# Kernel tuning notes

Measured on AMD Instinct MI355X. Metric: run time of the kernel, lower is better.

## Reference

```python
import jax, jax.numpy as jnp
import numpy as np

B, T, D, FF, H, K = 8, 1024, 512, 2048, 8, 15
HD = D // H  # key_dim = d_model // num_heads


def _ln(x, g, b):
    # keras LayerNormalization default epsilon = 1e-3
    m = jnp.mean(x, axis=-1, keepdims=True)
    v = jnp.var(x, axis=-1, keepdims=True)
    return (x - m) * jax.lax.rsqrt(v + 1e-3) * g + b


def setup_inputs() -> dict:
    key = jax.random.key(0)
    ks = iter(jax.random.split(key, 64))

    def rn(shape, s=0.02):
        return jax.random.normal(next(ks), shape, jnp.float32) * s

    p = {}
    p['x'] = jax.random.normal(next(ks), (B, T, D), jnp.float32)
    # ff_pre: LN -> Dense(FF, relu) -> Dense(D)
    p['g1'] = jnp.ones((D,), jnp.float32); p['b1'] = jnp.zeros((D,), jnp.float32)
    p['Wff1'] = rn((D, FF)); p['bff1'] = jnp.zeros((FF,), jnp.float32)
    p['Wff2'] = rn((FF, D)); p['bff2'] = jnp.zeros((D,), jnp.float32)
    # attention norm + MHA projections (keras EinsumDense shapes)
    p['ga'] = jnp.ones((D,), jnp.float32); p['ba'] = jnp.zeros((D,), jnp.float32)
    p['Wq'] = rn((D, H, HD)); p['bq'] = jnp.zeros((H, HD), jnp.float32)
    p['Wk'] = rn((D, H, HD)); p['bk'] = jnp.zeros((H, HD), jnp.float32)
    p['Wv'] = rn((D, H, HD)); p['bv'] = jnp.zeros((H, HD), jnp.float32)
    p['Wo'] = rn((H, HD, D)); p['bo'] = jnp.zeros((D,), jnp.float32)
    # conv branch: LN -> pointwise conv (2D, gelu) -> depthwise conv(k=15) -> BN -> swish -> pointwise conv (D)
    p['gc'] = jnp.ones((D,), jnp.float32); p['bc'] = jnp.zeros((D,), jnp.float32)
    p['Wcp'] = rn((D, 2 * D)); p['bcp'] = jnp.zeros((2 * D,), jnp.float32)
    p['dwk'] = rn((K, 1, 2 * D)); p['dwb'] = jnp.zeros((2 * D,), jnp.float32)
    p['bn_g'] = jnp.ones((2 * D,), jnp.float32); p['bn_b'] = jnp.zeros((2 * D,), jnp.float32)
    p['bn_m'] = jnp.zeros((2 * D,), jnp.float32)
    p['bn_v'] = jnp.ones((2 * D,), jnp.float32)
    p['Wco'] = rn((2 * D, D)); p['bco'] = jnp.zeros((D,), jnp.float32)
    # ff_post
    p['g2'] = jnp.ones((D,), jnp.float32); p['b2'] = jnp.zeros((D,), jnp.float32)
    p['Wf1'] = rn((D, FF)); p['bf1'] = jnp.zeros((FF,), jnp.float32)
    p['Wf2'] = rn((FF, D)); p['bf2'] = jnp.zeros((D,), jnp.float32)
    return p


def reference(x, g1, b1, Wff1, bff1, Wff2, bff2, ga, ba, Wq, bq, Wk, bk, Wv, bv, Wo, bo, gc, bc, Wcp, bcp, dwk, dwb, bn_g, bn_b, bn_m, bn_v, Wco, bco, g2, b2, Wf1, bf1, Wf2, bf2):
    # Macaron FFN (pre), half-step residual applied later
    x_ff = jnp.maximum(_ln(x, g1, b1) @ Wff1 + bff1, 0.0) @ Wff2 + bff2

    # causal multi-head self-attention (cache=None path)
    a = _ln(x, ga, ba)
    q = jnp.einsum('btd,dhk->bthk', a, Wq) + bq
    k = jnp.einsum('btd,dhk->bthk', a, Wk) + bk
    v = jnp.einsum('btd,dhk->bthk', a, Wv) + bv
    scores = jnp.einsum('bqhd,bkhd->bhqk', q, k) / jnp.sqrt(jnp.float32(HD))
    causal = jnp.tril(jnp.ones((T, T), bool))  # [T,T]
    scores = jnp.where(causal, scores, jnp.float32(-1e9))
    w = jax.nn.softmax(scores, axis=-1)
    ctx = jnp.einsum('bhqk,bkhd->bqhd', w, v)
    attn = jnp.einsum('bqhd,hdo->bqo', ctx, Wo) + bo

    x = x + 0.5 * x_ff + attn

    # convolution module: pointwise(gelu) -> causal left-pad -> depthwise -> BN(inference) -> swish -> pointwise
    c = jax.nn.gelu(_ln(x, gc, bc) @ Wcp + bcp, approximate=False)
    c = jnp.pad(c, ((0, 0), (K - 1, 0), (0, 0)))  # causal pad
    c = jax.lax.conv_general_dilated(
        c, dwk, window_strides=(1,), padding='VALID',
        dimension_numbers=('NWC', 'WIO', 'NWC'), feature_group_count=2 * D) + dwb
    c = (c - bn_m) * jax.lax.rsqrt(bn_v + 1e-3) * bn_g + bn_b
    c = c * jax.nn.sigmoid(c)  # swish
    c = c @ Wco + bco
    x = x + c

    # post FFN (full residual)
    x = x + (jnp.maximum(_ln(x, g2, b2) @ Wf1 + bf1, 0.0) @ Wf2 + bf2)
    return x
```

## Files before the change

### kernel.cpp

```cpp
#include <hip/hip_runtime.h>
#include <hip/hip_bf16.h>
#include <math.h>

#define BB 8
#define TT 1024
#define DD 512
#define FFD 2048
#define HH 8
#define HDD 64
#define KW 15
#define MR (BB*TT)
#define QKVN 1536

typedef __attribute__((ext_vector_type(8))) short short8;
typedef __attribute__((ext_vector_type(4))) short short4v;
typedef __attribute__((ext_vector_type(4))) float f32x4;
typedef __hip_bfloat16 bf16;

__device__ __forceinline__ float bf2f(unsigned u16) {
    return __uint_as_float(u16 << 16);
}

__device__ __forceinline__ void async_copy16(const void* g, void* l) {
    __builtin_amdgcn_global_load_lds(
        (const __attribute__((address_space(1))) void*)g,
        (__attribute__((address_space(3))) void*)l, 16, 0, 0);
}

__device__ __forceinline__ float gelu_exact(float v) {
    return 0.5f * v * (1.0f + erff(v * 0.70710678118654752f));
}

__global__ __launch_bounds__(256) void ln_dual_kernel(const float* __restrict__ x,
                                                      const float* __restrict__ g1,
                                                      const float* __restrict__ b1,
                                                      const float* __restrict__ ga,
                                                      const float* __restrict__ ba,
                                                      bf16* __restrict__ o1,
                                                      bf16* __restrict__ o2) {
    int wave = (blockIdx.x * blockDim.x + threadIdx.x) >> 6;
    int lane = threadIdx.x & 63;
    if (wave >= MR) return;
    const float* row = x + (size_t)wave * DD;
    float4 v0 = ((const float4*)row)[lane];
    float4 v1 = ((const float4*)row)[64 + lane];
    float s  = v0.x + v0.y + v0.z + v0.w + v1.x + v1.y + v1.z + v1.w;
    float ss = v0.x*v0.x + v0.y*v0.y + v0.z*v0.z + v0.w*v0.w
             + v1.x*v1.x + v1.y*v1.y + v1.z*v1.z + v1.w*v1.w;
    #pragma unroll
    for (int off = 32; off >= 1; off >>= 1) {
        s  += __shfl_xor(s,  off, 64);
        ss += __shfl_xor(ss, off, 64);
    }
    float mean = s * (1.0f / DD);
    float var  = ss * (1.0f / DD) - mean * mean;
    float r    = rsqrtf(var + 1e-3f);
    float n0x = (v0.x - mean) * r, n0y = (v0.y - mean) * r,
          n0z = (v0.z - mean) * r, n0w = (v0.w - mean) * r;
    float n1x = (v1.x - mean) * r, n1y = (v1.y - mean) * r,
          n1z = (v1.z - mean) * r, n1w = (v1.w - mean) * r;
    {
        float4 g0 = ((const float4*)g1)[lane];
        float4 gg1 = ((const float4*)g1)[64 + lane];
        float4 b0 = ((const float4*)b1)[lane];
        float4 bb1 = ((const float4*)b1)[64 + lane];
        alignas(8) bf16 oo0[4], oo1[4];
        oo0[0] = __float2bfloat16(n0x * g0.x + b0.x);
        oo0[1] = __float2bfloat16(n0y * g0.y + b0.y);
        oo0[2] = __float2bfloat16(n0z * g0.z + b0.z);
        oo0[3] = __float2bfloat16(n0w * g0.w + b0.w);
        oo1[0] = __float2bfloat16(n1x * gg1.x + bb1.x);
        oo1[1] = __float2bfloat16(n1y * gg1.y + bb1.y);
        oo1[2] = __float2bfloat16(n1z * gg1.z + bb1.z);
        oo1[3] = __float2bfloat16(n1w * gg1.w + bb1.w);
        bf16* orow = o1 + (size_t)wave * DD;
        *(short4v*)(orow + lane * 4)       = *(const short4v*)oo0;
        *(short4v*)(orow + 256 + lane * 4) = *(const short4v*)oo1;
    }
    {
        float4 g0 = ((const float4*)ga)[lane];
        float4 gg1 = ((const float4*)ga)[64 + lane];
        float4 b0 = ((const float4*)ba)[lane];
        float4 bb1 = ((const float4*)ba)[64 + lane];
        alignas(8) bf16 oo0[4], oo1[4];
        oo0[0] = __float2bfloat16(n0x * g0.x + b0.x);
        oo0[1] = __float2bfloat16(n0y * g0.y + b0.y);
        oo0[2] = __float2bfloat16(n0z * g0.z + b0.z);
        oo0[3] = __float2bfloat16(n0w * g0.w + b0.w);
        oo1[0] = __float2bfloat16(n1x * gg1.x + bb1.x);
        oo1[1] = __float2bfloat16(n1y * gg1.y + bb1.y);
        oo1[2] = __float2bfloat16(n1z * gg1.z + bb1.z);
        oo1[3] = __float2bfloat16(n1w * gg1.w + bb1.w);
        bf16* orow = o2 + (size_t)wave * DD;
        *(short4v*)(orow + lane * 4)       = *(const short4v*)oo0;
        *(short4v*)(orow + 256 + lane * 4) = *(const short4v*)oo1;
    }
}

__global__ __launch_bounds__(256) void ln_kernel(const float* __restrict__ x,
                                                 const float* __restrict__ g,
                                                 const float* __restrict__ b,
                                                 bf16* __restrict__ out) {
    int wave = (blockIdx.x * blockDim.x + threadIdx.x) >> 6;
    int lane = threadIdx.x & 63;
    if (wave >= MR) return;
    const float* row = x + (size_t)wave * DD;
    float4 v0 = ((const float4*)row)[lane];
    float4 v1 = ((const float4*)row)[64 + lane];
    float s  = v0.x + v0.y + v0.z + v0.w + v1.x + v1.y + v1.z + v1.w;
    float ss = v0.x*v0.x + v0.y*v0.y + v0.z*v0.z + v0.w*v0.w
             + v1.x*v1.x + v1.y*v1.y + v1.z*v1.z + v1.w*v1.w;
    #pragma unroll
    for (int off = 32; off >= 1; off >>= 1) {
        s  += __shfl_xor(s,  off, 64);
        ss += __shfl_xor(ss, off, 64);
    }
    float mean = s * (1.0f / DD);
    float var  = ss * (1.0f / DD) - mean * mean;
    float r    = rsqrtf(var + 1e-3f);
    float4 g0 = ((const float4*)g)[lane];
    float4 g1 = ((const float4*)g)[64 + lane];
    float4 b0 = ((const float4*)b)[lane];
    float4 b1 = ((const float4*)b)[64 + lane];
    alignas(8) bf16 o0[4], o1[4];
    o0[0] = __float2bfloat16((v0.x - mean) * r * g0.x + b0.x);
    o0[1] = __float2bfloat16((v0.y - mean) * r * g0.y + b0.y);
    o0[2] = __float2bfloat16((v0.z - mean) * r * g0.z + b0.z);
    o0[3] = __float2bfloat16((v0.w - mean) * r * g0.w + b0.w);
    o1[0] = __float2bfloat16((v1.x - mean) * r * g1.x + b1.x);
    o1[1] = __float2bfloat16((v1.y - mean) * r * g1.y + b1.y);
    o1[2] = __float2bfloat16((v1.z - mean) * r * g1.z + b1.z);
    o1[3] = __float2bfloat16((v1.w - mean) * r * g1.w + b1.w);
    bf16* orow = out + (size_t)wave * DD;
    *(short4v*)(orow + lane * 4)       = *(const short4v*)o0;
    *(short4v*)(orow + 256 + lane * 4) = *(const short4v*)o1;
}

struct WtPack {
    const float* src[10];
    bf16*        dst[10];
    int          K[10];
    int          lgNT[10];
    float        scale[10];
    int          off[10];
    const float* bq; const float* bk; const float* bv;
    float*       bdst;
};

__global__ __launch_bounds__(256) void wtrans_all_kernel(WtPack P) {
    __shared__ alignas(16) bf16 T[64][72];
    const int bid = blockIdx.x;
    if (bid >= 1536) {
        #pragma unroll
        for (int it = 0; it < 6; ++it) {
            int i = it * 256 + threadIdx.x;
            float v = i < 512 ? P.bq[i] * 0.125f
                              : (i < 1024 ? P.bk[i - 512] : P.bv[i - 1024]);
            P.bdst[i] = v;
        }
        return;
    }
    int e = 0;
    #pragma unroll
    for (int i = 1; i < 10; ++i) e = (bid >= P.off[i]) ? i : e;
    const float* W  = P.src[e];
    bf16*        Wt = P.dst[e];
    const int    K  = P.K[e];
    const int    lg = P.lgNT[e];
    const float  scale = P.scale[e];
    const int local = bid - P.off[e];
    const int bx = local & ((1 << lg) - 1);
    const int by = local >> lg;
    const int k0 = by * 64;
    const int n0 = bx * 64;
    const int N  = (1 << lg) * 64;
    const int tid = threadIdx.x;
    #pragma unroll
    for (int it = 0; it < 4; ++it) {
        int lin = it * 256 + tid;
        int kl  = lin >> 4;
        int nq  = (lin & 15) * 4;
        float4 v = *(const float4*)(W + (size_t)(k0 + kl) * N + n0 + nq);
        T[nq + 0][kl] = __float2bfloat16(v.x * scale);
        T[nq + 1][kl] = __float2bfloat16(v.y * scale);
        T[nq + 2][kl] = __float2bfloat16(v.z * scale);
        T[nq + 3][kl] = __float2bfloat16(v.w * scale);
    }
    __syncthreads();
    #pragma unroll
    for (int it = 0; it < 4; ++it) {
        int lin = it * 256 + tid;
        int nl  = lin >> 4;
        int kq  = (lin & 15) * 4;
        *(short4v*)(Wt + (size_t)(n0 + nl) * K + k0 + kq) = *(const short4v*)&T[nl][kq];
    }
}

template<int BN, int OP, int RESMODE, int OUTMODE>
__global__ __launch_bounds__(256) void bgemm_kernel(
    const bf16* __restrict__ A,
    const bf16* __restrict__ Bt,
    const float* __restrict__ bias,
    const float* __restrict__ res1,
    const bf16* __restrict__ res2,
    bf16* __restrict__ aux,
    float s2, float oscale,
    void* __restrict__ Cout,
    int N, int Kd, int nxb)
{
    constexpr int NT = BN / 32;
    __shared__ alignas(16) bf16 As[128][64];
    __shared__ alignas(16) bf16 Bs[BN][64];
    const int tid  = threadIdx.x;
    const int w    = tid >> 6;
    const int lane = tid & 63;
    const int quad = lane >> 4;
    const int l16  = lane & 15;
    const int wm   = w >> 1, wn = w & 1;

    const int flat = blockIdx.x;
    const int c8   = flat & 7;
    const int j    = flat >> 3;
    const int jy   = j / nxb;
    const int m0   = (c8 * 8 + jy) * 128;
    const int n0   = (j - jy * nxb) * BN;

    const int srow = lane >> 3;
    const int scol = ((lane & 7) ^ srow) * 8;

    const bf16* Ap = A  + (size_t)(m0 + w * 32 + srow) * Kd + scol;
    const bf16* Bp = Bt + (size_t)(n0 + w * (BN / 4) + srow) * Kd + scol;

    f32x4 acc[4][NT] = {};

    for (int k0 = 0; k0 < Kd; k0 += 64) {
        #pragma unroll
        for (int i = 0; i < 4; ++i)
            async_copy16(Ap + (size_t)(i * 8) * Kd + k0, &As[w * 32 + i * 8][0]);
        #pragma unroll
        for (int i = 0; i < BN / 32; ++i)
            async_copy16(Bp + (size_t)(i * 8) * Kd + k0, &Bs[w * (BN / 4) + i * 8][0]);
        __syncthreads();
        #pragma unroll
        for (int ks = 0; ks < 2; ++ks) {
            short8 af[4], bfr[NT];
            #pragma unroll
            for (int mt = 0; mt < 4; ++mt) {
                const int row = wm * 64 + mt * 16 + l16;
                const int c   = ((ks * 4 + quad) ^ (row & 7)) * 16;
                af[mt] = *(const short8*)((const char*)&As[row][0] + c);
            }
            #pragma unroll
            for (int nt = 0; nt < NT; ++nt) {
                const int col = wn * (BN / 2) + nt * 16 + l16;
                const int c   = ((ks * 4 + quad) ^ (col & 7)) * 16;
                bfr[nt] = *(const short8*)((const char*)&Bs[col][0] + c);
            }
            #pragma unroll
            for (int mt = 0; mt < 4; ++mt)
                #pragma unroll
                for (int nt = 0; nt < NT; ++nt)
                    acc[mt][nt] = __builtin_amdgcn_mfma_f32_16x16x32_bf16(
                        af[mt], bfr[nt], acc[mt][nt], 0, 0, 0);
        }
        __syncthreads();
    }

    const int crow0 = m0 + wm * 64 + quad * 4;
    const int ccol0 = n0 + wn * (BN / 2) + l16;
    #pragma unroll
    for (int nt = 0; nt < NT; ++nt) {
        const int col = ccol0 + nt * 16;
        const float bv = bias[col];
        #pragma unroll
        for (int mt = 0; mt < 4; ++mt) {
            if (OUTMODE == 2) {
                alignas(8) bf16 o4[4];
                #pragma unroll
                for (int r = 0; r < 4; ++r)
                    o4[r] = __float2bfloat16((acc[mt][nt][r] + bv) * oscale);
                if (col < 1024) {
                    #pragma unroll
                    for (int r = 0; r < 4; ++r)
                        ((bf16*)Cout)[(size_t)(crow0 + mt * 16 + r) * N + col] = o4[r];
                } else {
                    const int dg   = col - 1024;
                    const int rowt = crow0 + mt * 16;
                    const int b2   = rowt >> 10, t0 = rowt & 1023;
                    const int bh2  = b2 * 8 + (dg >> 6), d = dg & 63;
                    *(short4v*)(aux + ((size_t)bh2 * 64 + d) * TT + t0) =
                        *(const short4v*)o4;
                }
            } else {
                #pragma unroll
                for (int r = 0; r < 4; ++r) {
                    const int row = crow0 + mt * 16 + r;
                    const size_t off = (size_t)row * N + col;
                    float o = acc[mt][nt][r] + bv;
                    if (OP == 1)      o = fmaxf(o, 0.f);
                    else if (OP == 2) o = gelu_exact(o);
                    if (RESMODE >= 1) o += res1[off];
                    if (RESMODE == 2) o += s2 * __bfloat162float(res2[off]);
                    if (OUTMODE == 0) ((float*)Cout)[off] = o;
                    else              ((bf16*)Cout)[off]  = __float2bfloat16(o * oscale);
                }
            }
        }
    }
}

__global__ __launch_bounds__(256) void fattn_kernel(
    const bf16* __restrict__ QKV,
    const bf16* __restrict__ Vt,
    bf16* __restrict__ ctx)
{
    __shared__ alignas(16) bf16 Ks[2][64][64];
    __shared__ alignas(16) bf16 Vs[2][64][64];
    const int tid  = threadIdx.x;
    const int w    = tid >> 6;
    const int lane = tid & 63;
    const int quad = lane >> 4;
    const int l16  = lane & 15;
    const int bh   = blockIdx.x & 63;
    const int bi   = 7 - (blockIdx.x >> 6);
    const int b = bh >> 3, h = bh & 7;

    const bf16* Qg = QKV + (size_t)(b * TT) * QKVN + h * 64;
    const bf16* Kg = QKV + (size_t)(b * TT) * QKVN + 512 + h * 64;
    const bf16* Vg = Vt  + (size_t)bh * 64 * TT;

    const int qL = bi * 128 + w * 16;
    const int qH = qL + 64;
    short8 qfL0 = *(const short8*)(Qg + (size_t)(qL + l16) * QKVN + quad * 8);
    short8 qfL1 = *(const short8*)(Qg + (size_t)(qL + l16) * QKVN + 32 + quad * 8);
    short8 qfH0 = *(const short8*)(Qg + (size_t)(qH + l16) * QKVN + quad * 8);
    short8 qfH1 = *(const short8*)(Qg + (size_t)(qH + l16) * QKVN + 32 + quad * 8);

    const int sgrow  = lane >> 3;
    const int sgchnk = lane & 7;

    f32x4 caccL[4] = {}, caccH[4] = {};
    float lL = 0.f, lH = 0.f;
    const int prow_base = ((l16 >> 2) << 3) + (l16 & 3);
    const int smax = 2 * bi + 1;

    #pragma unroll
    for (int i = 0; i < 2; ++i) {
        const int rowbase = w * 8 + i * 32;
        const int row = rowbase + sgrow;
        const int fR = (row & 3) | (((row >> 3) & 1) << 2);
        const int sc = sgchnk ^ fR;
        async_copy16(Kg + (size_t)row * QKVN + sc * 8, &Ks[0][rowbase][0]);
        async_copy16(Vg + (size_t)row * TT + sc * 8,   &Vs[0][rowbase][0]);
    }

    int buf = 0;
    for (int s = 0; s <= smax; ++s) {
        __syncthreads();
        if (s < smax) {
            const int kn = (s + 1) * 64;
            #pragma unroll
            for (int i = 0; i < 2; ++i) {
                const int rowbase = w * 8 + i * 32;
                const int row = rowbase + sgrow;
                const int fR = (row & 3) | (((row >> 3) & 1) << 2);
                const int sc = sgchnk ^ fR;
                async_copy16(Kg + (size_t)(kn + row) * QKVN + sc * 8, &Ks[buf ^ 1][rowbase][0]);
                async_copy16(Vg + (size_t)row * TT + kn + sc * 8,     &Vs[buf ^ 1][rowbase][0]);
            }
        }
        const int k0 = s * 64;
        const bool doL = (s < smax);

        f32x4 sTL[4], sTH[4];
        #pragma unroll
        for (int s4 = 0; s4 < 4; ++s4) {
            const int prow = prow_base + (s4 >> 1) * 32 + (s4 & 1) * 4;
            const int fR = (prow & 3) | (((prow >> 3) & 1) << 2);
            short8 ka = *(const short8*)&Ks[buf][prow][(quad ^ fR) * 8];
            short8 kb = *(const short8*)&Ks[buf][prow][((4 + quad) ^ fR) * 8];
            f32x4 zH = {0.f, 0.f, 0.f, 0.f};
            zH = __builtin_amdgcn_mfma_f32_16x16x32_bf16(ka, qfH0, zH, 0, 0, 0);
            sTH[s4] = __builtin_amdgcn_mfma_f32_16x16x32_bf16(kb, qfH1, zH, 0, 0, 0);
            if (doL) {
                f32x4 zL = {0.f, 0.f, 0.f, 0.f};
                zL = __builtin_amdgcn_mfma_f32_16x16x32_bf16(ka, qfL0, zL, 0, 0, 0);
                sTL[s4] = __builtin_amdgcn_mfma_f32_16x16x32_bf16(kb, qfL1, zL, 0, 0, 0);
            }
        }

        alignas(16) bf16 pbH[16], pbL[16];
        if (s == smax) {
            const int qg = qH + l16;
            #pragma unroll
            for (int s4 = 0; s4 < 4; ++s4)
                #pragma unroll
                for (int r = 0; r < 4; ++r) {
                    const int key = k0 + (s4 >> 1) * 32 + quad * 8 + (s4 & 1) * 4 + r;
                    const float p = (key <= qg) ? __expf(sTH[s4][r]) : 0.f;
                    lH += p;
                    pbH[s4 * 4 + r] = __float2bfloat16(p);
                }
        } else {
            #pragma unroll
            for (int s4 = 0; s4 < 4; ++s4)
                #pragma unroll
                for (int r = 0; r < 4; ++r) {
                    const float p = __expf(sTH[s4][r]);
                    lH += p;
                    pbH[s4 * 4 + r] = __float2bfloat16(p);
                }
        }
        if (doL) {
            if (s == smax - 1) {
                const int qg = qL + l16;
                #pragma unroll
                for (int s4 = 0; s4 < 4; ++s4)
                    #pragma unroll
                    for (int r = 0; r < 4; ++r) {
                        const int key = k0 + (s4 >> 1) * 32 + quad * 8 + (s4 & 1) * 4 + r;
                        const float p = (key <= qg) ? __expf(sTL[s4][r]) : 0.f;
                        lL += p;
                        pbL[s4 * 4 + r] = __float2bfloat16(p);
                    }
            } else {
                #pragma unroll
                for (int s4 = 0; s4 < 4; ++s4)
                    #pragma unroll
                    for (int r = 0; r < 4; ++r) {
                        const float p = __expf(sTL[s4][r]);
                        lL += p;
                        pbL[s4 * 4 + r] = __float2bfloat16(p);
                    }
            }
        }
        const short8 pfH0 = *(const short8*)&pbH[0];
        const short8 pfH1 = *(const short8*)&pbH[8];
        const short8 pfL0 = *(const short8*)&pbL[0];
        const short8 pfL1 = *(const short8*)&pbL[8];

        #pragma unroll
        for (int g = 0; g < 4; ++g) {
            const int vrow = g * 16 + l16;
            const int fR = (vrow & 3) | (((vrow >> 3) & 1) << 2);
            short8 va = *(const short8*)&Vs[buf][vrow][(quad ^ fR) * 8];
            short8 vb = *(const short8*)&Vs[buf][vrow][((4 + quad) ^ fR) * 8];
            caccH[g] = __builtin_amdgcn_mfma_f32_16x16x32_bf16(va, pfH0, caccH[g], 0, 0, 0);
            caccH[g] = __builtin_amdgcn_mfma_f32_16x16x32_bf16(vb, pfH1, caccH[g], 0, 0, 0);
            if (doL) {
                caccL[g] = __builtin_amdgcn_mfma_f32_16x16x32_bf16(va, pfL0, caccL[g], 0, 0, 0);
                caccL[g] = __builtin_amdgcn_mfma_f32_16x16x32_bf16(vb, pfL1, caccL[g], 0, 0, 0);
            }
        }
        buf ^= 1;
    }

    lL += __shfl_xor(lL, 16, 64);
    lL += __shfl_xor(lL, 32, 64);
    lH += __shfl_xor(lH, 16, 64);
    lH += __shfl_xor(lH, 32, 64);
    const float invL = 1.0f / lL;
    const float invH = 1.0f / lH;

    bf16* CbL = ctx + (size_t)(b * TT + qL + l16) * DD + h * 64;
    bf16* CbH = ctx + (size_t)(b * TT + qH + l16) * DD + h * 64;
    #pragma unroll
    for (int g = 0; g < 4; ++g) {
        alignas(8) bf16 oL[4], oH[4];
        #pragma unroll
        for (int r = 0; r < 4; ++r) {
            oL[r] = __float2bfloat16(caccL[g][r] * invL);
            oH[r] = __float2bfloat16(caccH[g][r] * invH);
        }
        *(short4v*)(CbL + g * 16 + quad * 4) = *(const short4v*)oL;
        *(short4v*)(CbH + g * 16 + quad * 4) = *(const short4v*)oH;
    }
}

__global__ __launch_bounds__(256) void dwconv_kernel(const bf16* __restrict__ c1,
                                                     const float* __restrict__ dwk,
                                                     const float* __restrict__ dwb,
                                                     const float* __restrict__ bn_g,
                                                     const float* __restrict__ bn_b,
                                                     const float* __restrict__ bn_m,
                                                     const float* __restrict__ bn_v,
                                                     bf16* __restrict__ out) {
    const int C2 = 2 * DD;
    const int lin = blockIdx.x * 256 + threadIdx.x;
    const int chp = lin & 511;
    const int ch  = chp << 1;
    const int tch = lin >> 9;
    const int row0 = tch << 3;
    const int t0   = row0 & (TT - 1);

    float w0[KW], w1[KW];
    #pragma unroll
    for (int i = 0; i < KW; ++i) {
        w0[i] = dwk[i * C2 + ch];
        w1[i] = dwk[i * C2 + ch + 1];
    }
    const float a0 = rsqrtf(bn_v[ch] + 1e-3f) * bn_g[ch];
    const float a1 = rsqrtf(bn_v[ch + 1] + 1e-3f) * bn_g[ch + 1];
    const float c0 = (dwb[ch] - bn_m[ch]) * a0 + bn_b[ch];
    const float c1v = (dwb[ch + 1] - bn_m[ch + 1]) * a1 + bn_b[ch + 1];

    float x0[22], x1[22];
    if (t0 >= KW - 1) {
        #pragma unroll
        for (int i = 0; i < 22; ++i) {
            unsigned u = *(const unsigned*)(c1 + (size_t)(row0 - (KW - 1) + i) * C2 + ch);
            x0[i] = bf2f(u & 0xffff);
            x1[i] = bf2f(u >> 16);
        }
    } else {
        #pragma unroll
        for (int i = 0; i < 22; ++i) {
            unsigned u = 0;
            if (t0 - (KW - 1) + i >= 0)
                u = *(const unsigned*)(c1 + (size_t)(row0 - (KW - 1) + i) * C2 + ch);
            x0[i] = bf2f(u & 0xffff);
            x1[i] = bf2f(u >> 16);
        }
    }

    #pragma unroll
    for (int j = 0; j < 8; ++j) {
        float s0 = 0.f, s1 = 0.f;
        #pragma unroll
        for (int i = 0; i < KW; ++i) {
            s0 += x0[j + i] * w0[i];
            s1 += x1[j + i] * w1[i];
        }
        s0 = s0 * a0 + c0;
        s1 = s1 * a1 + c1v;
        s0 = s0 / (1.f + __expf(-s0));
        s1 = s1 / (1.f + __expf(-s1));
        alignas(4) bf16 ob[2] = {__float2bfloat16(s0), __float2bfloat16(s1)};
        *(unsigned*)(out + (size_t)(row0 + j) * C2 + ch) = *(const unsigned*)ob;
    }
}

extern "C" void kernel_launch(void* const* d_in, const int* in_sizes, int n_in,
                              void* d_out, int out_size, void* d_ws, size_t ws_size,
                              hipStream_t stream) {
    const float* x    = (const float*)d_in[0];
    const float* g1   = (const float*)d_in[1];
    const float* b1   = (const float*)d_in[2];
    const float* Wff1 = (const float*)d_in[3];
    const float* bff1 = (const float*)d_in[4];
    const float* Wff2 = (const float*)d_in[5];
    const float* bff2 = (const float*)d_in[6];
    const float* ga   = (const float*)d_in[7];
    const float* ba   = (const float*)d_in[8];
    const float* Wq   = (const float*)d_in[9];
    const float* bq   = (const float*)d_in[10];
    const float* Wk   = (const float*)d_in[11];
    const float* bk   = (const float*)d_in[12];
    const float* Wv   = (const float*)d_in[13];
    const float* bv   = (const float*)d_in[14];
    const float* Wo   = (const float*)d_in[15];
    const float* bo   = (const float*)d_in[16];
    const float* gc   = (const float*)d_in[17];
    const float* bc   = (const float*)d_in[18];
    const float* Wcp  = (const float*)d_in[19];
    const float* bcp  = (const float*)d_in[20];
    const float* dwk  = (const float*)d_in[21];
    const float* dwb  = (const float*)d_in[22];
    const float* bn_g = (const float*)d_in[23];
    const float* bn_b = (const float*)d_in[24];
    const float* bn_m = (const float*)d_in[25];
    const float* bn_v = (const float*)d_in[26];
    const float* Wco  = (const float*)d_in[27];
    const float* bco  = (const float*)d_in[28];
    const float* g2   = (const float*)d_in[29];
    const float* b2   = (const float*)d_in[30];
    const float* Wf1  = (const float*)d_in[31];
    const float* bf1  = (const float*)d_in[32];
    const float* Wf2  = (const float*)d_in[33];
    const float* bf2  = (const float*)d_in[34];

    float* out = (float*)d_out;

    char* p = (char*)d_ws;
    bf16* lnb   = (bf16*)p;  p += (size_t)MR * DD * 2;
    bf16* lnab  = (bf16*)p;  p += (size_t)MR * DD * 2;
    bf16* qkvb  = (bf16*)p;  p += (size_t)MR * QKVN * 2;
    bf16* Vtb   = (bf16*)p;  p += (size_t)MR * DD * 2;
    bf16* ctxb  = (bf16*)p;  p += (size_t)MR * DD * 2;
    bf16* xffb  = (bf16*)p;  p += (size_t)MR * DD * 2;
    bf16* bigb  = (bf16*)p;  p += (size_t)MR * FFD * 2;
    bf16* c2b   = (bf16*)p;  p += (size_t)MR * 1024 * 2;
    bf16* Wff1t = (bf16*)p;  p += (size_t)FFD * DD * 2;
    bf16* Wff2t = (bf16*)p;  p += (size_t)DD * FFD * 2;
    bf16* Wqkvt = (bf16*)p;  p += (size_t)QKVN * DD * 2;
    bf16* Wot   = (bf16*)p;  p += (size_t)DD * DD * 2;
    bf16* Wcpt  = (bf16*)p;  p += (size_t)1024 * DD * 2;
    bf16* Wcot  = (bf16*)p;  p += (size_t)DD * 1024 * 2;
    bf16* Wf1t  = (bf16*)p;  p += (size_t)FFD * DD * 2;
    bf16* Wf2t  = (bf16*)p;  p += (size_t)DD * FFD * 2;
    float* bqkv = (float*)p; p += QKVN * 4;

    dim3 blk(256);
    dim3 ln_grid(MR / 4);

    WtPack P;
    auto set = [&](int i, const float* s, bf16* d, int K, int N, float sc, int off) {
        P.src[i] = s; P.dst[i] = d; P.K[i] = K; P.scale[i] = sc; P.off[i] = off;
        int nt = N / 64, lg = 0; while ((1 << lg) < nt) ++lg; P.lgNT[i] = lg;
    };
    set(0, Wff1, Wff1t, DD,  FFD, 1.f,    0);
    set(1, Wff2, Wff2t, FFD, DD,  1.f,    256);
    set(2, Wq,   Wqkvt,                DD, DD, 0.125f, 512);
    set(3, Wk,   Wqkvt + (size_t)512 * DD,  DD, DD, 1.f, 576);
    set(4, Wv,   Wqkvt + (size_t)1024 * DD, DD, DD, 1.f, 640);
    set(5, Wo,   Wot,   DD,  DD,  1.f,    704);
    set(6, Wcp,  Wcpt,  DD,  1024, 1.f,   768);
    set(7, Wco,  Wcot,  1024, DD, 1.f,    896);
    set(8, Wf1,  Wf1t,  DD,  FFD, 1.f,    1024);
    set(9, Wf2,  Wf2t,  FFD, DD,  1.f,    1280);
    P.bq = bq; P.bk = bk; P.bv = bv; P.bdst = bqkv;
    wtrans_all_kernel<<<dim3(1537), blk, 0, stream>>>(P);

    ln_dual_kernel<<<ln_grid, blk, 0, stream>>>(x, g1, b1, ga, ba, lnb, lnab);
    bgemm_kernel<128, 1, 0, 1><<<dim3(16 * 64), blk, 0, stream>>>(
        lnb, Wff1t, bff1, nullptr, nullptr, nullptr, 0.f, 1.f, bigb, FFD, DD, 16);
    bgemm_kernel<64, 0, 0, 1><<<dim3(8 * 64), blk, 0, stream>>>(
        bigb, Wff2t, bff2, nullptr, nullptr, nullptr, 0.f, 1.f, xffb, DD, FFD, 8);
    bgemm_kernel<128, 0, 0, 2><<<dim3(12 * 64), blk, 0, stream>>>(
        lnab, Wqkvt, bqkv, nullptr, nullptr, Vtb, 0.f, 1.f, qkvb, QKVN, DD, 12);
    fattn_kernel<<<dim3(64 * 8), blk, 0, stream>>>(qkvb, Vtb, ctxb);
    bgemm_kernel<64, 0, 2, 0><<<dim3(8 * 64), blk, 0, stream>>>(
        ctxb, Wot, bo, x, xffb, nullptr, 0.5f, 1.f, out, DD, DD, 8);
    ln_kernel<<<ln_grid, blk, 0, stream>>>(out, gc, bc, lnb);
    bgemm_kernel<128, 2, 0, 1><<<dim3(8 * 64), blk, 0, stream>>>(
        lnb, Wcpt, bcp, nullptr, nullptr, nullptr, 0.f, 1.f, bigb, 1024, DD, 8);
    dwconv_kernel<<<dim3(MR * 512 / 8 / 256), blk, 0, stream>>>(
        bigb, dwk, dwb, bn_g, bn_b, bn_m, bn_v, c2b);
    bgemm_kernel<64, 0, 1, 0><<<dim3(8 * 64), blk, 0, stream>>>(
        c2b, Wcot, bco, out, nullptr, nullptr, 0.f, 1.f, out, DD, 1024, 8);
    ln_kernel<<<ln_grid, blk, 0, stream>>>(out, g2, b2, lnb);
    bgemm_kernel<128, 1, 0, 1><<<dim3(16 * 64), blk, 0, stream>>>(
        lnb, Wf1t, bf1, nullptr, nullptr, nullptr, 0.f, 1.f, bigb, FFD, DD, 16);
    bgemm_kernel<64, 0, 1, 0><<<dim3(8 * 64), blk, 0, stream>>>(
        bigb, Wf2t, bf2, out, nullptr, nullptr, 0.f, 1.f, out, DD, FFD, 8);
}
```

Before: 394.7 us.

## Merge independent stages into combined multi-job kernels to cut launches and idle tails

Folds the dual LayerNorm into the weight-transpose prep kernel and runs FF1 and QKV GEMMs in one launch by splitting blocks by index. It also runs the FF2 GEMM alongside flash attention in one kernel. Independent work can then fill the device together and fewer launches occur. The cost is heterogeneous blocks sharing one register and LDS budget, which may lower occupancy for the attention and GEMM paths.

```diff
diff --git a/kernel.cpp b/kernel.cpp
--- a/kernel.cpp
+++ b/kernel.cpp
@@ -31,112 +31,7 @@
     return 0.5f * v * (1.0f + erff(v * 0.70710678118654752f));
 }
 
-__global__ __launch_bounds__(256) void ln_dual_kernel(const float* __restrict__ x,
-                                                      const float* __restrict__ g1,
-                                                      const float* __restrict__ b1,
-                                                      const float* __restrict__ ga,
-                                                      const float* __restrict__ ba,
-                                                      bf16* __restrict__ o1,
-                                                      bf16* __restrict__ o2) {
-    int wave = (blockIdx.x * blockDim.x + threadIdx.x) >> 6;
-    int lane = threadIdx.x & 63;
-    if (wave >= MR) return;
-    const float* row = x + (size_t)wave * DD;
-    float4 v0 = ((const float4*)row)[lane];
-    float4 v1 = ((const float4*)row)[64 + lane];
-    float s  = v0.x + v0.y + v0.z + v0.w + v1.x + v1.y + v1.z + v1.w;
-    float ss = v0.x*v0.x + v0.y*v0.y + v0.z*v0.z + v0.w*v0.w
-             + v1.x*v1.x + v1.y*v1.y + v1.z*v1.z + v1.w*v1.w;
-    #pragma unroll
-    for (int off = 32; off >= 1; off >>= 1) {
-        s  += __shfl_xor(s,  off, 64);
-        ss += __shfl_xor(ss, off, 64);
-    }
-    float mean = s * (1.0f / DD);
-    float var  = ss * (1.0f / DD) - mean * mean;
-    float r    = rsqrtf(var + 1e-3f);
-    float n0x = (v0.x - mean) * r, n0y = (v0.y - mean) * r,
-          n0z = (v0.z - mean) * r, n0w = (v0.w - mean) * r;
-    float n1x = (v1.x - mean) * r, n1y = (v1.y - mean) * r,
-          n1z = (v1.z - mean) * r, n1w = (v1.w - mean) * r;
-    {
-        float4 g0 = ((const float4*)g1)[lane];
-        float4 gg1 = ((const float4*)g1)[64 + lane];
-        float4 b0 = ((const float4*)b1)[lane];
-        float4 bb1 = ((const float4*)b1)[64 + lane];
-        alignas(8) bf16 oo0[4], oo1[4];
-        oo0[0] = __float2bfloat16(n0x * g0.x + b0.x);
-        oo0[1] = __float2bfloat16(n0y * g0.y + b0.y);
-        oo0[2] = __float2bfloat16(n0z * g0.z + b0.z);
-        oo0[3] = __float2bfloat16(n0w * g0.w + b0.w);
-        oo1[0] = __float2bfloat16(n1x * gg1.x + bb1.x);
-        oo1[1] = __float2bfloat16(n1y * gg1.y + bb1.y);
-        oo1[2] = __float2bfloat16(n1z * gg1.z + bb1.z);
-        oo1[3] = __float2bfloat16(n1w * gg1.w + bb1.w);
-        bf16* orow = o1 + (size_t)wave * DD;
-        *(short4v*)(orow + lane * 4)       = *(const short4v*)oo0;
-        *(short4v*)(orow + 256 + lane * 4) = *(const short4v*)oo1;
-    }
-    {
-        float4 g0 = ((const float4*)ga)[lane];
-        float4 gg1 = ((const float4*)ga)[64 + lane];
-        float4 b0 = ((const float4*)ba)[lane];
-        float4 bb1 = ((const float4*)ba)[64 + lane];
-        alignas(8) bf16 oo0[4], oo1[4];
-        oo0[0] = __float2bfloat16(n0x * g0.x + b0.x);
-        oo0[1] = __float2bfloat16(n0y * g0.y + b0.y);
-        oo0[2] = __float2bfloat16(n0z * g0.z + b0.z);
-        oo0[3] = __float2bfloat16(n0w * g0.w + b0.w);
-        oo1[0] = __float2bfloat16(n1x * gg1.x + bb1.x);
-        oo1[1] = __float2bfloat16(n1y * gg1.y + bb1.y);
-        oo1[2] = __float2bfloat16(n1z * gg1.z + bb1.z);
-        oo1[3] = __float2bfloat16(n1w * gg1.w + bb1.w);
-        bf16* orow = o2 + (size_t)wave * DD;
-        *(short4v*)(orow + lane * 4)       = *(const short4v*)oo0;
-        *(short4v*)(orow + 256 + lane * 4) = *(const short4v*)oo1;
-    }
-}
-
-__global__ __launch_bounds__(256) void ln_kernel(const float* __restrict__ x,
-                                                 const float* __restrict__ g,
-                                                 const float* __restrict__ b,
-                                                 bf16* __restrict__ out) {
-    int wave = (blockIdx.x * blockDim.x + threadIdx.x) >> 6;
-    int lane = threadIdx.x & 63;
-    if (wave >= MR) return;
-    const float* row = x + (size_t)wave * DD;
-    float4 v0 = ((const float4*)row)[lane];
-    float4 v1 = ((const float4*)row)[64 + lane];
-    float s  = v0.x + v0.y + v0.z + v0.w + v1.x + v1.y + v1.z + v1.w;
-    float ss = v0.x*v0.x + v0.y*v0.y + v0.z*v0.z + v0.w*v0.w
-             + v1.x*v1.x + v1.y*v1.y + v1.z*v1.z + v1.w*v1.w;
-    #pragma unroll
-    for (int off = 32; off >= 1; off >>= 1) {
-        s  += __shfl_xor(s,  off, 64);
-        ss += __shfl_xor(ss, off, 64);
-    }
-    float mean = s * (1.0f / DD);
-    float var  = ss * (1.0f / DD) - mean * mean;
-    float r    = rsqrtf(var + 1e-3f);
-    float4 g0 = ((const float4*)g)[lane];
-    float4 g1 = ((const float4*)g)[64 + lane];
-    float4 b0 = ((const float4*)b)[lane];
-    float4 b1 = ((const float4*)b)[64 + lane];
-    alignas(8) bf16 o0[4], o1[4];
-    o0[0] = __float2bfloat16((v0.x - mean) * r * g0.x + b0.x);
-    o0[1] = __float2bfloat16((v0.y - mean) * r * g0.y + b0.y);
-    o0[2] = __float2bfloat16((v0.z - mean) * r * g0.z + b0.z);
-    o0[3] = __float2bfloat16((v0.w - mean) * r * g0.w + b0.w);
-    o1[0] = __float2bfloat16((v1.x - mean) * r * g1.x + b1.x);
-    o1[1] = __float2bfloat16((v1.y - mean) * r * g1.y + b1.y);
-    o1[2] = __float2bfloat16((v1.z - mean) * r * g1.z + b1.z);
-    o1[3] = __float2bfloat16((v1.w - mean) * r * g1.w + b1.w);
-    bf16* orow = out + (size_t)wave * DD;
-    *(short4v*)(orow + lane * 4)       = *(const short4v*)o0;
-    *(short4v*)(orow + 256 + lane * 4) = *(const short4v*)o1;
-}
-
-struct WtPack {
+struct PrepPack {
     const float* src[10];
     bf16*        dst[10];
     int          K[10];
@@ -145,18 +40,80 @@
     int          off[10];
     const float* bq; const float* bk; const float* bv;
     float*       bdst;
+    const float* x;
+    const float* g1; const float* b1; const float* ga; const float* ba;
+    bf16* o1; bf16* o2;
 };
 
-__global__ __launch_bounds__(256) void wtrans_all_kernel(WtPack P) {
+__global__ __launch_bounds__(256) void prep_kernel(PrepPack P) {
     __shared__ alignas(16) bf16 T[64][72];
     const int bid = blockIdx.x;
-    if (bid >= 1536) {
+    if (bid == 1536) {
         #pragma unroll
         for (int it = 0; it < 6; ++it) {
             int i = it * 256 + threadIdx.x;
             float v = i < 512 ? P.bq[i] * 0.125f
                               : (i < 1024 ? P.bk[i - 512] : P.bv[i - 1024]);
             P.bdst[i] = v;
+        }
+        return;
+    }
+    if (bid > 1536) {
+        int wave = ((bid - 1537) * 256 + (int)threadIdx.x) >> 6;
+        int lane = threadIdx.x & 63;
+        const float* row = P.x + (size_t)wave * DD;
+        float4 v0 = ((const float4*)row)[lane];
+        float4 v1 = ((const float4*)row)[64 + lane];
+        float s  = v0.x + v0.y + v0.z + v0.w + v1.x + v1.y + v1.z + v1.w;
+        float ss = v0.x*v0.x + v0.y*v0.y + v0.z*v0.z + v0.w*v0.w
+                 + v1.x*v1.x + v1.y*v1.y + v1.z*v1.z + v1.w*v1.w;
+        #pragma unroll
+        for (int off = 32; off >= 1; off >>= 1) {
+            s  += __shfl_xor(s,  off, 64);
+            ss += __shfl_xor(ss, off, 64);
+        }
+        float mean = s * (1.0f / DD);
+        float var  = ss * (1.0f / DD) - mean * mean;
+        float r    = rsqrtf(var + 1e-3f);
+        float n0x = (v0.x - mean) * r, n0y = (v0.y - mean) * r,
+              n0z = (v0.z - mean) * r, n0w = (v0.w - mean) * r;
+        float n1x = (v1.x - mean) * r, n1y = (v1.y - mean) * r,
+              n1z = (v1.z - mean) * r, n1w = (v1.w - mean) * r;
+        {
+            float4 g0 = ((const float4*)P.g1)[lane];
+            float4 gg = ((const float4*)P.g1)[64 + lane];
+            float4 b0 = ((const float4*)P.b1)[lane];
+            float4 bb = ((const float4*)P.b1)[64 + lane];
+            alignas(8) bf16 o0[4], o1[4];
+            o0[0] = __float2bfloat16(n0x * g0.x + b0.x);
+            o0[1] = __float2bfloat16(n0y * g0.y + b0.y);
+            o0[2] = __float2bfloat16(n0z * g0.z + b0.z);
+            o0[3] = __float2bfloat16(n0w * g0.w + b0.w);
+            o1[0] = __float2bfloat16(n1x * gg.x + bb.x);
+            o1[1] = __float2bfloat16(n1y * gg.y + bb.y);
+            o1[2] = __float2bfloat16(n1z * gg.z + bb.z);
+            o1[3] = __float2bfloat16(n1w * gg.w + bb.w);
+            bf16* orow = P.o1 + (size_t)wave * DD;
+            *(short4v*)(orow + lane * 4)       = *(const short4v*)o0;
+            *(short4v*)(orow + 256 + lane * 4) = *(const short4v*)o1;
+        }
+        {
+            float4 g0 = ((const float4*)P.ga)[lane];
+            float4 gg = ((const float4*)P.ga)[64 + lane];
+            float4 b0 = ((const float4*)P.ba)[lane];
+            float4 bb = ((const float4*)P.ba)[64 + lane];
+            alignas(8) bf16 o0[4], o1[4];
+            o0[0] = __float2bfloat16(n0x * g0.x + b0.x);
+            o0[1] = __float2bfloat16(n0y * g0.y + b0.y);
+            o0[2] = __float2bfloat16(n0z * g0.z + b0.z);
+            o0[3] = __float2bfloat16(n0w * g0.w + b0.w);
+            o1[0] = __float2bfloat16(n1x * gg.x + bb.x);
+            o1[1] = __float2bfloat16(n1y * gg.y + bb.y);
+            o1[2] = __float2bfloat16(n1z * gg.z + bb.z);
+            o1[3] = __float2bfloat16(n1w * gg.w + bb.w);
+            bf16* orow = P.o2 + (size_t)wave * DD;
+            *(short4v*)(orow + lane * 4)       = *(const short4v*)o0;
+            *(short4v*)(orow + 256 + lane * 4) = *(const short4v*)o1;
         }
         return;
     }
@@ -196,6 +153,45 @@
     }
 }
 
+__global__ __launch_bounds__(256) void ln_kernel(const float* __restrict__ x,
+                                                 const float* __restrict__ g,
+                                                 const float* __restrict__ b,
+                                                 bf16* __restrict__ out) {
+    int wave = (blockIdx.x * blockDim.x + threadIdx.x) >> 6;
+    int lane = threadIdx.x & 63;
+    if (wave >= MR) return;
+    const float* row = x + (size_t)wave * DD;
+    float4 v0 = ((const float4*)row)[lane];
+    float4 v1 = ((const float4*)row)[64 + lane];
+    float s  = v0.x + v0.y + v0.z + v0.w + v1.x + v1.y + v1.z + v1.w;
+    float ss = v0.x*v0.x + v0.y*v0.y + v0.z*v0.z + v0.w*v0.w
+             + v1.x*v1.x + v1.y*v1.y + v1.z*v1.z + v1.w*v1.w;
+    #pragma unroll
+    for (int off = 32; off >= 1; off >>= 1) {
+        s  += __shfl_xor(s,  off, 64);
+        ss += __shfl_xor(ss, off, 64);
+    }
+    float mean = s * (1.0f / DD);
+    float var  = ss * (1.0f / DD) - mean * mean;
+    float r    = rsqrtf(var + 1e-3f);
+    float4 g0 = ((const float4*)g)[lane];
+    float4 g1 = ((const float4*)g)[64 + lane];
+    float4 b0 = ((const float4*)b)[lane];
+    float4 b1 = ((const float4*)b)[64 + lane];
+    alignas(8) bf16 o0[4], o1[4];
+    o0[0] = __float2bfloat16((v0.x - mean) * r * g0.x + b0.x);
+    o0[1] = __float2bfloat16((v0.y - mean) * r * g0.y + b0.y);
+    o0[2] = __float2bfloat16((v0.z - mean) * r * g0.z + b0.z);
+    o0[3] = __float2bfloat16((v0.w - mean) * r * g0.w + b0.w);
+    o1[0] = __float2bfloat16((v1.x - mean) * r * g1.x + b1.x);
+    o1[1] = __float2bfloat16((v1.y - mean) * r * g1.y + b1.y);
+    o1[2] = __float2bfloat16((v1.z - mean) * r * g1.z + b1.z);
+    o1[3] = __float2bfloat16((v1.w - mean) * r * g1.w + b1.w);
+    bf16* orow = out + (size_t)wave * DD;
+    *(short4v*)(orow + lane * 4)       = *(const short4v*)o0;
+    *(short4v*)(orow + 256 + lane * 4) = *(const short4v*)o1;
+}
+
 template<int BN, int OP, int RESMODE, int OUTMODE>
 __global__ __launch_bounds__(256) void bgemm_kernel(
     const bf16* __restrict__ A,
@@ -203,7 +199,6 @@
     const float* __restrict__ bias,
     const float* __restrict__ res1,
     const bf16* __restrict__ res2,
-    bf16* __restrict__ aux,
     float s2, float oscale,
     void* __restrict__ Cout,
     int N, int Kd, int nxb)
@@ -274,206 +269,370 @@
         const float bv = bias[col];
         #pragma unroll
         for (int mt = 0; mt < 4; ++mt) {
-            if (OUTMODE == 2) {
-                alignas(8) bf16 o4[4];
-                #pragma unroll
-                for (int r = 0; r < 4; ++r)
-                    o4[r] = __float2bfloat16((acc[mt][nt][r] + bv) * oscale);
-                if (col < 1024) {
-                    #pragma unroll
-                    for (int r = 0; r < 4; ++r)
-                        ((bf16*)Cout)[(size_t)(crow0 + mt * 16 + r) * N + col] = o4[r];
-                } else {
-                    const int dg   = col - 1024;
-                    const int rowt = crow0 + mt * 16;
-                    const int b2   = rowt >> 10, t0 = rowt & 1023;
-                    const int bh2  = b2 * 8 + (dg >> 6), d = dg & 63;
-                    *(short4v*)(aux + ((size_t)bh2 * 64 + d) * TT + t0) =
-                        *(const short4v*)o4;
-                }
-            } else {
-                #pragma unroll
-                for (int r = 0; r < 4; ++r) {
-                    const int row = crow0 + mt * 16 + r;
-                    const size_t off = (size_t)row * N + col;
-                    float o = acc[mt][nt][r] + bv;
-                    if (OP == 1)      o = fmaxf(o, 0.f);
-                    else if (OP == 2) o = gelu_exact(o);
-                    if (RESMODE >= 1) o += res1[off];
-                    if (RESMODE == 2) o += s2 * __bfloat162float(res2[off]);
-                    if (OUTMODE == 0) ((float*)Cout)[off] = o;
-                    else              ((bf16*)Cout)[off]  = __float2bfloat16(o * oscale);
-                }
-            }
-        }
-    }
-}
-
-__global__ __launch_bounds__(256) void fattn_kernel(
-    const bf16* __restrict__ QKV,
-    const bf16* __restrict__ Vt,
-    bf16* __restrict__ ctx)
+            #pragma unroll
+            for (int r = 0; r < 4; ++r) {
+                const int row = crow0 + mt * 16 + r;
+                const size_t off = (size_t)row * N + col;
+                float o = acc[mt][nt][r] + bv;
+                if (OP == 1)      o = fmaxf(o, 0.f);
+                else if (OP == 2) o = gelu_exact(o);
+                if (RESMODE >= 1) o += res1[off];
+                if (RESMODE == 2) o += s2 * __bfloat162float(res2[off]);
+                if (OUTMODE == 0) ((float*)Cout)[off] = o;
+                else              ((bf16*)Cout)[off]  = __float2bfloat16(o * oscale);
+            }
+        }
+    }
+}
+
+__global__ __launch_bounds__(256) void ffqkv_kernel(
+    const bf16* __restrict__ lnb, const bf16* __restrict__ lnab,
+    const bf16* __restrict__ Wff1t, const bf16* __restrict__ Wqkvt,
+    const float* __restrict__ bff1, const float* __restrict__ bqkv,
+    bf16* __restrict__ bigb, bf16* __restrict__ qkvb, bf16* __restrict__ Vtb)
 {
-    __shared__ alignas(16) bf16 Ks[2][64][64];
-    __shared__ alignas(16) bf16 Vs[2][64][64];
+    __shared__ alignas(16) bf16 As[128][64];
+    __shared__ alignas(16) bf16 Bs[128][64];
     const int tid  = threadIdx.x;
     const int w    = tid >> 6;
     const int lane = tid & 63;
     const int quad = lane >> 4;
     const int l16  = lane & 15;
-    const int bh   = blockIdx.x & 63;
-    const int bi   = 7 - (blockIdx.x >> 6);
-    const int b = bh >> 3, h = bh & 7;
-
-    const bf16* Qg = QKV + (size_t)(b * TT) * QKVN + h * 64;
-    const bf16* Kg = QKV + (size_t)(b * TT) * QKVN + 512 + h * 64;
-    const bf16* Vg = Vt  + (size_t)bh * 64 * TT;
-
-    const int qL = bi * 128 + w * 16;
-    const int qH = qL + 64;
-    short8 qfL0 = *(const short8*)(Qg + (size_t)(qL + l16) * QKVN + quad * 8);
-    short8 qfL1 = *(const short8*)(Qg + (size_t)(qL + l16) * QKVN + 32 + quad * 8);
-    short8 qfH0 = *(const short8*)(Qg + (size_t)(qH + l16) * QKVN + quad * 8);
-    short8 qfH1 = *(const short8*)(Qg + (size_t)(qH + l16) * QKVN + 32 + quad * 8);
-
-    const int sgrow  = lane >> 3;
-    const int sgchnk = lane & 7;
-
-    f32x4 caccL[4] = {}, caccH[4] = {};
-    float lL = 0.f, lH = 0.f;
-    const int prow_base = ((l16 >> 2) << 3) + (l16 & 3);
-    const int smax = 2 * bi + 1;
-
+    const int wm   = w >> 1, wn = w & 1;
+
+    const bool jobq = blockIdx.x >= 1024;
+    const int  flat = jobq ? (int)blockIdx.x - 1024 : (int)blockIdx.x;
+    const int  nxb  = jobq ? 12 : 16;
+    const int  N    = jobq ? QKVN : FFD;
+    const bf16* A   = jobq ? lnab : lnb;
+    const bf16* Bt  = jobq ? Wqkvt : Wff1t;
+    const float* bias = jobq ? bqkv : bff1;
+
+    const int c8 = flat & 7;
+    const int j  = flat >> 3;
+    const int jy = j / nxb;
+    const int m0 = (c8 * 8 + jy) * 128;
+    const int n0 = (j - jy * nxb) * 128;
+
+    const int srow = lane >> 3;
+    const int scol = ((lane & 7) ^ srow) * 8;
+
+    const bf16* Ap = A  + (size_t)(m0 + w * 32 + srow) * DD + scol;
+    const bf16* Bp = Bt + (size_t)(n0 + w * 32 + srow) * DD + scol;
+
+    f32x4 acc[4][4] = {};
+
+    for (int k0 = 0; k0 < DD; k0 += 64) {
+        #pragma unroll
+        for (int i = 0; i < 4; ++i) {
+            async_copy16(Ap + (size_t)(i * 8) * DD + k0, &As[w * 32 + i * 8][0]);
+            async_copy16(Bp + (size_t)(i * 8) * DD + k0, &Bs[w * 32 + i * 8][0]);
+        }
+        __syncthreads();
+        #pragma unroll
+        for (int ks = 0; ks < 2; ++ks) {
+            short8 af[4], bfr[4];
+            #pragma unroll
+            for (int mt = 0; mt < 4; ++mt) {
+                const int row = wm * 64 + mt * 16 + l16;
+                const int c   = ((ks * 4 + quad) ^ (row & 7)) * 16;
+                af[mt] = *(const short8*)((const char*)&As[row][0] + c);
+            }
+            #pragma unroll
+            for (int nt = 0; nt < 4; ++nt) {
+                const int col = wn * 64 + nt * 16 + l16;
+                const int c   = ((ks * 4 + quad) ^ (col & 7)) * 16;
+                bfr[nt] = *(const short8*)((const char*)&Bs[col][0] + c);
+            }
+            #pragma unroll
+            for (int mt = 0; mt < 4; ++mt)
+                #pragma unroll
+                for (int nt = 0; nt < 4; ++nt)
+                    acc[mt][nt] = __builtin_amdgcn_mfma_f32_16x16x32_bf16(
+                        af[mt], bfr[nt], acc[mt][nt], 0, 0, 0);
+        }
+        __syncthreads();
+    }
+
+    const int crow0 = m0 + wm * 64 + quad * 4;
+    const int ccol0 = n0 + wn * 64 + l16;
     #pragma unroll
-    for (int i = 0; i < 2; ++i) {
-        const int rowbase = w * 8 + i * 32;
-        const int row = rowbase + sgrow;
-        const int fR = (row & 3) | (((row >> 3) & 1) << 2);
-        const int sc = sgchnk ^ fR;
-        async_copy16(Kg + (size_t)row * QKVN + sc * 8, &Ks[0][rowbase][0]);
-        async_copy16(Vg + (size_t)row * TT + sc * 8,   &Vs[0][rowbase][0]);
-    }
-
-    int buf = 0;
-    for (int s = 0; s <= smax; ++s) {
-        __syncthreads();
-        if (s < smax) {
-            const int kn = (s + 1) * 64;
-            #pragma unroll
-            for (int i = 0; i < 2; ++i) {
-                const int rowbase = w * 8 + i * 32;
-                const int row = rowbase + sgrow;
-                const int fR = (row & 3) | (((row >> 3) & 1) << 2);
-                const int sc = sgchnk ^ fR;
-                async_copy16(Kg + (size_t)(kn + row) * QKVN + sc * 8, &Ks[buf ^ 1][rowbase][0]);
-                async_copy16(Vg + (size_t)row * TT + kn + sc * 8,     &Vs[buf ^ 1][rowbase][0]);
-            }
-        }
-        const int k0 = s * 64;
-        const bool doL = (s < smax);
-
-        f32x4 sTL[4], sTH[4];
-        #pragma unroll
-        for (int s4 = 0; s4 < 4; ++s4) {
-            const int prow = prow_base + (s4 >> 1) * 32 + (s4 & 1) * 4;
-            const int fR = (prow & 3) | (((prow >> 3) & 1) << 2);
-            short8 ka = *(const short8*)&Ks[buf][prow][(quad ^ fR) * 8];
-            short8 kb = *(const short8*)&Ks[buf][prow][((4 + quad) ^ fR) * 8];
-            f32x4 zH = {0.f, 0.f, 0.f, 0.f};
-            zH = __builtin_amdgcn_mfma_f32_16x16x32_bf16(ka, qfH0, zH, 0, 0, 0);
-            sTH[s4] = __builtin_amdgcn_mfma_f32_16x16x32_bf16(kb, qfH1, zH, 0, 0, 0);
-            if (doL) {
-                f32x4 zL = {0.f, 0.f, 0.f, 0.f};
-                zL = __builtin_amdgcn_mfma_f32_16x16x32_bf16(ka, qfL0, zL, 0, 0, 0);
-                sTL[s4] = __builtin_amdgcn_mfma_f32_16x16x32_bf16(kb, qfL1, zL, 0, 0, 0);
-            }
-        }
-
-        alignas(16) bf16 pbH[16], pbL[16];
-        if (s == smax) {
-            const int qg = qH + l16;
-            #pragma unroll
-            for (int s4 = 0; s4 < 4; ++s4)
+    for (int nt = 0; nt < 4; ++nt) {
+        const int col = ccol0 + nt * 16;
+        const float bv = bias[col];
+        #pragma unroll
+        for (int mt = 0; mt < 4; ++mt) {
+            if (jobq) {
+                alignas(8) bf16 o4[4];
+                #pragma unroll
+                for (int r = 0; r < 4; ++r)
+                    o4[r] = __float2bfloat16(acc[mt][nt][r] + bv);
+                if (col < 1024) {
+                    #pragma unroll
+                    for (int r = 0; r < 4; ++r)
+                        qkvb[(size_t)(crow0 + mt * 16 + r) * QKVN + col] = o4[r];
+                } else {
+                    const int dg   = col - 1024;
+                    const int rowt = crow0 + mt * 16;
+                    const int bb   = rowt >> 10, t0 = rowt & 1023;
+                    const int bh2  = bb * 8 + (dg >> 6), d = dg & 63;
+                    *(short4v*)(Vtb + ((size_t)bh2 * 64 + d) * TT + t0) =
+                        *(const short4v*)o4;
+                }
+            } else {
                 #pragma unroll
                 for (int r = 0; r < 4; ++r) {
-                    const int key = k0 + (s4 >> 1) * 32 + quad * 8 + (s4 & 1) * 4 + r;
-                    const float p = (key <= qg) ? __expf(sTH[s4][r]) : 0.f;
-                    lH += p;
-                    pbH[s4 * 4 + r] = __float2bfloat16(p);
+                    const float o = fmaxf(acc[mt][nt][r] + bv, 0.f);
+                    bigb[(size_t)(crow0 + mt * 16 + r) * FFD + col] =
+                        __float2bfloat16(o);
                 }
-        } else {
-            #pragma unroll
-            for (int s4 = 0; s4 < 4; ++s4)
-                #pragma unroll
-                for (int r = 0; r < 4; ++r) {
-                    const float p = __expf(sTH[s4][r]);
-                    lH += p;
-                    pbH[s4 * 4 + r] = __float2bfloat16(p);
+            }
+        }
+    }
+}
+
+__global__ __launch_bounds__(256) void ff2attn_kernel(
+    const bf16* __restrict__ QKV, const bf16* __restrict__ Vt,
+    bf16* __restrict__ ctx,
+    const bf16* __restrict__ bigb, const bf16* __restrict__ Wff2t,
+    const float* __restrict__ bff2, bf16* __restrict__ xffb)
+{
+    __shared__ alignas(16) bf16 smem[16384];
+    const int tid  = threadIdx.x;
+    const int w    = tid >> 6;
+    const int lane = tid & 63;
+    const int quad = lane >> 4;
+    const int l16  = lane & 15;
+
+    if (blockIdx.x < 512) {
+        typedef bf16 (*tile_t)[64][64];
+        tile_t Ks = (tile_t)smem;
+        tile_t Vs = (tile_t)(smem + 2 * 64 * 64);
+        const int bh = blockIdx.x & 63;
+        const int bi = 7 - ((int)blockIdx.x >> 6);
+        const int b = bh >> 3, h = bh & 7;
+
+        const bf16* Qg = QKV + (size_t)(b * TT) * QKVN + h * 64;
+        const bf16* Kg = QKV + (size_t)(b * TT) * QKVN + 512 + h * 64;
+        const bf16* Vg = Vt  + (size_t)bh * 64 * TT;
+
+        const int qL = bi * 128 + w * 16;
+        const int qH = qL + 64;
+        short8 qfL0 = *(const short8*)(Qg + (size_t)(qL + l16) * QKVN + quad * 8);
+        short8 qfL1 = *(const short8*)(Qg + (size_t)(qL + l16) * QKVN + 32 + quad * 8);
+        short8 qfH0 = *(const short8*)(Qg + (size_t)(qH + l16) * QKVN + quad * 8);
+        short8 qfH1 = *(const short8*)(Qg + (size_t)(qH + l16) * QKVN + 32 + quad * 8);
+
+        const int sgrow  = lane >> 3;
+        const int sgchnk = lane & 7;
+
+        f32x4 caccL[4] = {}, caccH[4] = {};
+        float lL = 0.f, lH = 0.f;
+        const int prow_base = ((l16 >> 2) << 3) + (l16 & 3);
+        const int smax = 2 * bi + 1;
+
+        #pragma unroll
+        for (int i = 0; i < 2; ++i) {
+            const int rowbase = w * 8 + i * 32;
+            const int row = rowbase + sgrow;
+            const int fR = (row & 3) | (((row >> 3) & 1) << 2);
+            const int sc = sgchnk ^ fR;
+            async_copy16(Kg + (size_t)row * QKVN + sc * 8, &Ks[0][rowbase][0]);
+            async_copy16(Vg + (size_t)row * TT + sc * 8,   &Vs[0][rowbase][0]);
+        }
+
+        int buf = 0;
+        for (int s = 0; s <= smax; ++s) {
+            __syncthreads();
+            if (s < smax) {
+                const int kn = (s + 1) * 64;
+                #pragma unroll
+                for (int i = 0; i < 2; ++i) {
+                    const int rowbase = w * 8 + i * 32;
+                    const int row = rowbase + sgrow;
+                    const int fR = (row & 3) | (((row >> 3) & 1) << 2);
+                    const int sc = sgchnk ^ fR;
+                    async_copy16(Kg + (size_t)(kn + row) * QKVN + sc * 8,
+                                 &Ks[buf ^ 1][rowbase][0]);
+                    async_copy16(Vg + (size_t)row * TT + kn + sc * 8,
+                                 &Vs[buf ^ 1][rowbase][0]);
                 }
-        }
-        if (doL) {
-            if (s == smax - 1) {
-                const int qg = qL + l16;
+            }
+            const int k0 = s * 64;
+            const bool doL = (s < smax);
+
+            f32x4 sTL[4], sTH[4];
+            #pragma unroll
+            for (int s4 = 0; s4 < 4; ++s4) {
+                const int prow = prow_base + (s4 >> 1) * 32 + (s4 & 1) * 4;
+                const int fR = (prow & 3) | (((prow >> 3) & 1) << 2);
+                short8 ka = *(const short8*)&Ks[buf][prow][(quad ^ fR) * 8];
+                short8 kb = *(const short8*)&Ks[buf][prow][((4 + quad) ^ fR) * 8];
+                f32x4 zH = {0.f, 0.f, 0.f, 0.f};
+                zH = __builtin_amdgcn_mfma_f32_16x16x32_bf16(ka, qfH0, zH, 0, 0, 0);
+                sTH[s4] = __builtin_amdgcn_mfma_f32_16x16x32_bf16(kb, qfH1, zH, 0, 0, 0);
+                if (doL) {
+                    f32x4 zL = {0.f, 0.f, 0.f, 0.f};
+                    zL = __builtin_amdgcn_mfma_f32_16x16x32_bf16(ka, qfL0, zL, 0, 0, 0);
+                    sTL[s4] = __builtin_amdgcn_mfma_f32_16x16x32_bf16(kb, qfL1, zL, 0, 0, 0);
+                }
+            }
+
+            alignas(16) bf16 pbH[16], pbL[16];
+            if (s == smax) {
+                const int qg = qH + l16;
                 #pragma unroll
                 for (int s4 = 0; s4 < 4; ++s4)
                     #pragma unroll
                     for (int r = 0; r < 4; ++r) {
                         const int key = k0 + (s4 >> 1) * 32 + quad * 8 + (s4 & 1) * 4 + r;
-                        const float p = (key <= qg) ? __expf(sTL[s4][r]) : 0.f;
-                        lL += p;
-                        pbL[s4 * 4 + r] = __float2bfloat16(p);
+                        const float p = (key <= qg) ? __expf(sTH[s4][r]) : 0.f;
+                        lH += p;
+                        pbH[s4 * 4 + r] = __float2bfloat16(p);
                     }
             } else {
                 #pragma unroll
                 for (int s4 = 0; s4 < 4; ++s4)
                     #pragma unroll
                     for (int r = 0; r < 4; ++r) {
-                        const float p = __expf(sTL[s4][r]);
-                        lL += p;
-                        pbL[s4 * 4 + r] = __float2bfloat16(p);
+                        const float p = __expf(sTH[s4][r]);
+                        lH += p;
+                        pbH[s4 * 4 + r] = __float2bfloat16(p);
                     }
             }
-        }
-        const short8 pfH0 = *(const short8*)&pbH[0];
-        const short8 pfH1 = *(const short8*)&pbH[8];
-        const short8 pfL0 = *(const short8*)&pbL[0];
-        const short8 pfL1 = *(const short8*)&pbL[8];
-
+            if (doL) {
+                if (s == smax - 1) {
+                    const int qg = qL + l16;
+                    #pragma unroll
+                    for (int s4 = 0; s4 < 4; ++s4)
+                        #pragma unroll
+                        for (int r = 0; r < 4; ++r) {
+                            const int key = k0 + (s4 >> 1) * 32 + quad * 8 + (s4 & 1) * 4 + r;
+                            const float p = (key <= qg) ? __expf(sTL[s4][r]) : 0.f;
+                            lL += p;
+                            pbL[s4 * 4 + r] = __float2bfloat16(p);
+                        }
+                } else {
+                    #pragma unroll
+                    for (int s4 = 0; s4 < 4; ++s4)
+                        #pragma unroll
+                        for (int r = 0; r < 4; ++r) {
+                            const float p = __expf(sTL[s4][r]);
+                            lL += p;
+                            pbL[s4 * 4 + r] = __float2bfloat16(p);
+                        }
+                }
+            }
+            const short8 pfH0 = *(const short8*)&pbH[0];
+            const short8 pfH1 = *(const short8*)&pbH[8];
+            const short8 pfL0 = *(const short8*)&pbL[0];
+            const short8 pfL1 = *(const short8*)&pbL[8];
+
+            #pragma unroll
+            for (int g = 0; g < 4; ++g) {
+                const int vrow = g * 16 + l16;
+                const int fR = (vrow & 3) | (((vrow >> 3) & 1) << 2);
+                short8 va = *(const short8*)&Vs[buf][vrow][(quad ^ fR) * 8];
+                short8 vb = *(const short8*)&Vs[buf][vrow][((4 + quad) ^ fR) * 8];
+                caccH[g] = __builtin_amdgcn_mfma_f32_16x16x32_bf16(va, pfH0, caccH[g], 0, 0, 0);
+                caccH[g] = __builtin_amdgcn_mfma_f32_16x16x32_bf16(vb, pfH1, caccH[g], 0, 0, 0);
+                if (doL) {
+                    caccL[g] = __builtin_amdgcn_mfma_f32_16x16x32_bf16(va, pfL0, caccL[g], 0, 0, 0);
+                    caccL[g] = __builtin_amdgcn_mfma_f32_16x16x32_bf16(vb, pfL1, caccL[g], 0, 0, 0);
+                }
+            }
+            buf ^= 1;
+        }
+
+        lL += __shfl_xor(lL, 16, 64);
+        lL += __shfl_xor(lL, 32, 64);
+        lH += __shfl_xor(lH, 16, 64);
+        lH += __shfl_xor(lH, 32, 64);
+        const float invL = 1.0f / lL;
+        const float invH = 1.0f / lH;
+
+        bf16* CbL = ctx + (size_t)(b * TT + qL + l16) * DD + h * 64;
+        bf16* CbH = ctx + (size_t)(b * TT + qH + l16) * DD + h * 64;
         #pragma unroll
         for (int g = 0; g < 4; ++g) {
-            const int vrow = g * 16 + l16;
-            const int fR = (vrow & 3) | (((vrow >> 3) & 1) << 2);
-            short8 va = *(const short8*)&Vs[buf][vrow][(quad ^ fR) * 8];
-            short8 vb = *(const short8*)&Vs[buf][vrow][((4 + quad) ^ fR) * 8];
-            caccH[g] = __builtin_amdgcn_mfma_f32_16x16x32_bf16(va, pfH0, caccH[g], 0, 0, 0);
-            caccH[g] = __builtin_amdgcn_mfma_f32_16x16x32_bf16(vb, pfH1, caccH[g], 0, 0, 0);
-            if (doL) {
-                caccL[g] = __builtin_amdgcn_mfma_f32_16x16x32_bf16(va, pfL0, caccL[g], 0, 0, 0);
-                caccL[g] = __builtin_amdgcn_mfma_f32_16x16x32_bf16(vb, pfL1, caccL[g], 0, 0, 0);
-            }
-        }
-        buf ^= 1;
-    }
-
-    lL += __shfl_xor(lL, 16, 64);
-    lL += __shfl_xor(lL, 32, 64);
-    lH += __shfl_xor(lH, 16, 64);
-    lH += __shfl_xor(lH, 32, 64);
-    const float invL = 1.0f / lL;
-    const float invH = 1.0f / lH;
-
-    bf16* CbL = ctx + (size_t)(b * TT + qL + l16) * DD + h * 64;
-    bf16* CbH = ctx + (size_t)(b * TT + qH + l16) * DD + h * 64;
-    #pragma unroll
-    for (int g = 0; g < 4; ++g) {
-        alignas(8) bf16 oL[4], oH[4];
-        #pragma unroll
-        for (int r = 0; r < 4; ++r) {
-            oL[r] = __float2bfloat16(caccL[g][r] * invL);
-            oH[r] = __float2bfloat16(caccH[g][r] * invH);
-        }
-        *(short4v*)(CbL + g * 16 + quad * 4) = *(const short4v*)oL;
-        *(short4v*)(CbH + g * 16 + quad * 4) = *(const short4v*)oH;
+            alignas(8) bf16 oL[4], oH[4];
+            #pragma unroll
+            for (int r = 0; r < 4; ++r) {
+                oL[r] = __float2bfloat16(caccL[g][r] * invL);
+                oH[r] = __float2bfloat16(caccH[g][r] * invH);
+            }
+            *(short4v*)(CbL + g * 16 + quad * 4) = *(const short4v*)oL;
+            *(short4v*)(CbH + g * 16 + quad * 4) = *(const short4v*)oH;
+        }
+    } else {
+        typedef bf16 (*row_t)[64];
+        row_t As = (row_t)smem;
+        row_t Bs = (row_t)(smem + 128 * 64);
+        const int wm = w >> 1, wn = w & 1;
+
+        const int flat = (int)blockIdx.x - 512;
+        const int c8 = flat & 7;
+        const int j  = flat >> 3;
+        const int jy = j >> 3;
+        const int m0 = (c8 * 8 + jy) * 128;
+        const int n0 = (j & 7) * 64;
+
+        const int srow = lane >> 3;
+        const int scol = ((lane & 7) ^ srow) * 8;
+
+        const bf16* Ap = bigb  + (size_t)(m0 + w * 32 + srow) * FFD + scol;
+        const bf16* Bp = Wff2t + (size_t)(n0 + w * 16 + srow) * FFD + scol;
+
+        f32x4 acc[4][2] = {};
+
+        for (int k0 = 0; k0 < FFD; k0 += 64) {
+            #pragma unroll
+            for (int i = 0; i < 4; ++i)
+                async_copy16(Ap + (size_t)(i * 8) * FFD + k0, &As[w * 32 + i * 8][0]);
+            #pragma unroll
+            for (int i = 0; i < 2; ++i)
+                async_copy16(Bp + (size_t)(i * 8) * FFD + k0, &Bs[w * 16 + i * 8][0]);
+            __syncthreads();
+            #pragma unroll
+            for (int ks = 0; ks < 2; ++ks) {
+                short8 af[4], bfr[2];
+                #pragma unroll
+                for (int mt = 0; mt < 4; ++mt) {
+                    const int row = wm * 64 + mt * 16 + l16;
+                    const int c   = ((ks * 4 + quad) ^ (row & 7)) * 16;
+                    af[mt] = *(const short8*)((const char*)&As[row][0] + c);
+                }
+                #pragma unroll
+                for (int nt = 0; nt < 2; ++nt) {
+                    const int col = wn * 32 + nt * 16 + l16;
+                    const int c   = ((ks * 4 + quad) ^ (col & 7)) * 16;
+                    bfr[nt] = *(const short8*)((const char*)&Bs[col][0] + c);
+                }
+                #pragma unroll
+                for (int mt = 0; mt < 4; ++mt)
+                    #pragma unroll
+                    for (int nt = 0; nt < 2; ++nt)
+                        acc[mt][nt] = __builtin_amdgcn_mfma_f32_16x16x32_bf16(
+                            af[mt], bfr[nt], acc[mt][nt], 0, 0, 0);
+            }
+            __syncthreads();
+        }
+
+        const int crow0 = m0 + wm * 64 + quad * 4;
+        const int ccol0 = n0 + wn * 32 + l16;
+        #pragma unroll
+        for (int nt = 0; nt < 2; ++nt) {
+            const int col = ccol0 + nt * 16;
+            const float bv = bff2[col];
+            #pragma unroll
+            for (int mt = 0; mt < 4; ++mt)
+                #pragma unroll
+                for (int r = 0; r < 4; ++r) {
+                    const int row = crow0 + mt * 16 + r;
+                    xffb[(size_t)row * DD + col] =
+                        __float2bfloat16(acc[mt][nt][r] + bv);
+                }
+        }
     }
 }
 
@@ -601,9 +760,8 @@
     float* bqkv = (float*)p; p += QKVN * 4;
 
     dim3 blk(256);
-    dim3 ln_grid(MR / 4);
-
-    WtPack P;
+
+    PrepPack P;
     auto set = [&](int i, const float* s, bf16* d, int K, int N, float sc, int off) {
         P.src[i] = s; P.dst[i] = d; P.K[i] = K; P.scale[i] = sc; P.off[i] = off;
         int nt = N / 64, lg = 0; while ((1 << lg) < nt) ++lg; P.lgNT[i] = lg;
@@ -619,28 +777,26 @@
     set(8, Wf1,  Wf1t,  DD,  FFD, 1.f,    1024);
     set(9, Wf2,  Wf2t,  FFD, DD,  1.f,    1280);
     P.bq = bq; P.bk = bk; P.bv = bv; P.bdst = bqkv;
-    wtrans_all_kernel<<<dim3(1537), blk, 0, stream>>>(P);
-
-    ln_dual_kernel<<<ln_grid, blk, 0, stream>>>(x, g1, b1, ga, ba, lnb, lnab);
-    bgemm_kernel<128, 1, 0, 1><<<dim3(16 * 64), blk, 0, stream>>>(
-        lnb, Wff1t, bff1, nullptr, nullptr, nullptr, 0.f, 1.f, bigb, FFD, DD, 16);
-    bgemm_kernel<64, 0, 0, 1><<<dim3(8 * 64), blk, 0, stream>>>(
-        bigb, Wff2t, bff2, nullptr, nullptr, nullptr, 0.f, 1.f, xffb, DD, FFD, 8);
-    bgemm_kernel<128, 0, 0, 2><<<dim3(12 * 64), blk, 0, stream>>>(
-        lnab, Wqkvt, bqkv, nullptr, nullptr, Vtb, 0.f, 1.f, qkvb, QKVN, DD, 12);
-    fattn_kernel<<<dim3(64 * 8), blk, 0, stream>>>(qkvb, Vtb, ctxb);
+    P.x = x; P.g1 = g1; P.b1 = b1; P.ga = ga; P.ba = ba;
+    P.o1 = lnb; P.o2 = lnab;
+
+    prep_kernel<<<dim3(1537 + MR / 4), blk, 0, stream>>>(P);
+    ffqkv_kernel<<<dim3(1024 + 768), blk, 0, stream>>>(
+        lnb, lnab, Wff1t, Wqkvt, bff1, bqkv, bigb, qkvb, Vtb);
+    ff2attn_kernel<<<dim3(1024), blk, 0, stream>>>(
+        qkvb, Vtb, ctxb, bigb, Wff2t, bff2, xffb);
     bgemm_kernel<64, 0, 2, 0><<<dim3(8 * 64), blk, 0, stream>>>(
-        ctxb, Wot, bo, x, xffb, nullptr, 0.5f, 1.f, out, DD, DD, 8);
-    ln_kernel<<<ln_grid, blk, 0, stream>>>(out, gc, bc, lnb);
+        ctxb, Wot, bo, x, xffb, 0.5f, 1.f, out, DD, DD, 8);
+    ln_kernel<<<dim3(MR / 4), blk, 0, stream>>>(out, gc, bc, lnb);
     bgemm_kernel<128, 2, 0, 1><<<dim3(8 * 64), blk, 0, stream>>>(
-        lnb, Wcpt, bcp, nullptr, nullptr, nullptr, 0.f, 1.f, bigb, 1024, DD, 8);
+        lnb, Wcpt, bcp, nullptr, nullptr, 0.f, 1.f, bigb, 1024, DD, 8);
     dwconv_kernel<<<dim3(MR * 512 / 8 / 256), blk, 0, stream>>>(
         bigb, dwk, dwb, bn_g, bn_b, bn_m, bn_v, c2b);
     bgemm_kernel<64, 0, 1, 0><<<dim3(8 * 64), blk, 0, stream>>>(
-        c2b, Wcot, bco, out, nullptr, nullptr, 0.f, 1.f, out, DD, 1024, 8);
-    ln_kernel<<<ln_grid, blk, 0, stream>>>(out, g2, b2, lnb);
+        c2b, Wcot, bco, out, nullptr, 0.f, 1.f, out, DD, 1024, 8);
+    ln_kernel<<<dim3(MR / 4), blk, 0, stream>>>(out, g2, b2, lnb);
     bgemm_kernel<128, 1, 0, 1><<<dim3(16 * 64), blk, 0, stream>>>(
-        lnb, Wf1t, bf1, nullptr, nullptr, nullptr, 0.f, 1.f, bigb, FFD, DD, 16);
+        lnb, Wf1t, bf1, nullptr, nullptr, 0.f, 1.f, bigb, FFD, DD, 16);
     bgemm_kernel<64, 0, 1, 0><<<dim3(8 * 64), blk, 0, stream>>>(
-        bigb, Wf2t, bf2, out, nullptr, nullptr, 0.f, 1.f, out, DD, FFD, 8);
-}
+        bigb, Wf2t, bf2, out, nullptr, 0.f, 1.f, out, DD, FFD, 8);
+}
```

Result: faster. 385.7 us (-2.3%).
